# Kernel tuning notes

Measured on AMD Instinct MI355X. Metric: run time of the kernel, lower is better.

## Reference

```python
import jax, jax.numpy as jnp
import numpy as np

N_HIDDEN = 256
BATCH, T, N_FEAT = 256, 512, 64


def setup_inputs() -> dict:
    key = jax.random.key(0)
    ks = jax.random.split(key, 10)
    s = lambda fan_in: 1.0 / np.sqrt(fan_in)
    return {
        "x": jax.random.normal(ks[0], (BATCH, T, N_FEAT), dtype=jnp.float32),
        # input-side Dense gates (with bias)
        "Wr": jax.random.normal(ks[1], (N_FEAT, N_HIDDEN), dtype=jnp.float32) * s(N_FEAT),
        "br": jnp.zeros((N_HIDDEN,), dtype=jnp.float32),
        "Wz": jax.random.normal(ks[2], (N_FEAT, N_HIDDEN), dtype=jnp.float32) * s(N_FEAT),
        "bz": jnp.zeros((N_HIDDEN,), dtype=jnp.float32),
        "Wg": jax.random.normal(ks[3], (N_FEAT, N_HIDDEN), dtype=jnp.float32) * s(N_FEAT),
        "bg": jnp.zeros((N_HIDDEN,), dtype=jnp.float32),
        # hidden-side Dense gates (no bias)
        "Hr": jax.random.normal(ks[4], (N_HIDDEN, N_HIDDEN), dtype=jnp.float32) * s(N_HIDDEN),
        "Hz": jax.random.normal(ks[5], (N_HIDDEN, N_HIDDEN), dtype=jnp.float32) * s(N_HIDDEN),
        "Hg": jax.random.normal(ks[6], (N_HIDDEN, N_HIDDEN), dtype=jnp.float32) * s(N_HIDDEN),
    }


def _gru_forward(x, Wr, br, Wz, bz, Wg, bg, Hr, Hz, Hg):
    B, T, _ = x.shape
    nh = Hr.shape[0]
    # Source loops for t in range(T-1), so only x[:, :T-1] is consumed.
    xs = x[:, : T - 1]
    # Batch all input-side projections across time (parallel part).
    ar = jnp.einsum("btf,fh->tbh", xs, Wr) + br  # [T-1, B, H]
    az = jnp.einsum("btf,fh->tbh", xs, Wz) + bz
    ag = jnp.einsum("btf,fh->tbh", xs, Wg) + bg

    h0 = jnp.zeros((B, nh), dtype=x.dtype)

    def step(h, gates):
        gr, gz, gg = gates
        rt = jax.nn.sigmoid(gr + h @ Hr)
        zt = jax.nn.sigmoid(gz + h @ Hz)
        gt = jnp.tanh(gg + (rt * h) @ Hg)
        h_new = (1.0 - zt) * h + zt * gt
        return h_new, h_new

    _, hs = jax.lax.scan(step, h0, (ar, az, ag))  # hs: [T-1, B, H]
    # Output list starts with the zero initial state, matching the source.
    out = jnp.concatenate([h0[None], hs], axis=0)  # [T, B, H]
    return jnp.transpose(out, (1, 0, 2))  # [B, T, H]


def reference(x, Wr, br, Wz, bz, Wg, bg, Hr, Hz, Hg):
    return _gru_forward(x, Wr, br, Wz, bz, Wg, bg, Hr, Hz, Hg)
```

## Files before the change

kernel.cpp:

```cpp
#include <hip/hip_runtime.h>
#include <hip/hip_bf16.h>


typedef _Float16 f16;
typedef _Float16 half8 __attribute__((ext_vector_type(8)));
typedef float floatx4 __attribute__((ext_vector_type(4)));

#define MFMA16(a, b, c) __builtin_amdgcn_mfma_f32_16x16x32_f16((a), (b), (c), 0, 0, 0)

#define WTAB_OFF   0u
#define RZTAB_OFF  98304u
#define GTAB_OFF   360448u
#define PRE_OFF    491520u
#define WS_NEED    (491520ull + 200933376ull)

__global__ void gru_wprep(const float* __restrict__ Wr, const float* __restrict__ Wz,
                          const float* __restrict__ Wg, const float* __restrict__ Hr,
                          const float* __restrict__ Hz, const float* __restrict__ Hg,
                          f16* __restrict__ ws) {
    int idx = blockIdx.x * 256 + threadIdx.x;
    if (idx >= 30720) return;
    const float* src;
    int col, k0;
    f16* dst;
    if (idx < 6144) {
        int lane = idx & 63, ktx = (idx >> 6) & 1, nt = (idx >> 7) & 15, g = idx >> 11;
        src = (g == 0) ? Wr : (g == 1) ? Wz : Wg;
        col = nt * 16 + (lane & 15);
        k0  = ktx * 32 + (lane >> 4) * 8;
        dst = ws + WTAB_OFF / 2 + (size_t)idx * 8;
    } else if (idx < 22528) {
        int local = idx - 6144;
        int kt = local & 7, nti = (local >> 3) & 1, g = (local >> 4) & 1, tid = local >> 5;
        int w = tid >> 6, l = tid & 63;
        src = g ? Hz : Hr;
        col = (w * 2 + nti) * 16 + (l & 15);
        k0  = kt * 32 + (l >> 4) * 8;
        dst = ws + RZTAB_OFF / 2 + (size_t)local * 8;
    } else {
        int local = idx - 22528;
        int lane = local & 63, q = local >> 6;
        int kt = q & 7, nt = q >> 3;
        src = Hg;
        col = nt * 16 + (lane & 15);
        k0  = kt * 32 + (lane >> 4) * 8;
        dst = ws + GTAB_OFF / 2 + (size_t)local * 8;
    }
    half8 v;
#pragma unroll
    for (int i = 0; i < 8; ++i) v[i] = (f16)src[(size_t)(k0 + i) * 256 + col];
    *(half8*)dst = v;
}

__global__ void __launch_bounds__(512)
gru_gates(const float* __restrict__ x, const float* __restrict__ br,
          const float* __restrict__ bz, const float* __restrict__ bg,
          f16* __restrict__ ws) {
    const int bid = blockIdx.x;
    const int t = bid >> 4, blk = bid & 15;
    const int tid = threadIdx.x, w = tid >> 6, l = tid & 63;
    const int cl = l & 15, rq = l >> 4;

    half8 xa[2];
    const float* xr = x + (size_t)(blk * 16 + cl) * 32768 + (size_t)t * 64 + rq * 8;
#pragma unroll
    for (int ktx = 0; ktx < 2; ++ktx) {
        float4 a = *(const float4*)(xr + ktx * 32);
        float4 b = *(const float4*)(xr + ktx * 32 + 4);
        half8 v;
        v[0] = (f16)a.x; v[1] = (f16)a.y; v[2] = (f16)a.z; v[3] = (f16)a.w;
        v[4] = (f16)b.x; v[5] = (f16)b.y; v[6] = (f16)b.z; v[7] = (f16)b.w;
        xa[ktx] = v;
    }

    const half8* Wt = (const half8*)(ws + WTAB_OFF / 2);
    floatx4 acc[3][2];
#pragma unroll
    for (int g = 0; g < 3; ++g)
#pragma unroll
        for (int nti = 0; nti < 2; ++nti) {
            int col = (w * 2 + nti) * 16 + cl;
            float b = (g == 0 ? br : g == 1 ? bz : bg)[col];
            acc[g][nti] = (floatx4){b, b, b, b};
        }
#pragma unroll
    for (int g = 0; g < 3; ++g)
#pragma unroll
        for (int nti = 0; nti < 2; ++nti) {
            int nt = w * 2 + nti;
#pragma unroll
            for (int ktx = 0; ktx < 2; ++ktx)
                acc[g][nti] = MFMA16(xa[ktx], Wt[(size_t)((g * 16 + nt) * 2 + ktx) * 64 + l],
                                     acc[g][nti]);
        }

    half8* preb = (half8*)(ws + PRE_OFF / 2);
#pragma unroll
    for (int g = 0; g < 3; ++g) {
        half8 v;
#pragma unroll
        for (int nti = 0; nti < 2; ++nti)
#pragma unroll
            for (int j = 0; j < 4; ++j)
                v[nti * 4 + j] = (f16)acc[g][nti][j];
        preb[((size_t)bid * 3 + g) * 512 + tid] = v;
    }
}

__global__ void __launch_bounds__(512, 2)
gru_scan3(const f16* __restrict__ ws, float* __restrict__ out) {
    extern __shared__ unsigned char smem[];
    unsigned char* sH  = smem;
    unsigned char* sRH = smem + 8192;
    unsigned char* sG  = smem + 16384;

    const int tid = threadIdx.x, w = tid >> 6, l = tid & 63;
    const int cl = l & 15, rq = l >> 4;
    const int blk = blockIdx.x, b0 = blk * 16;

    half8 rz[2][2][8];
    {
        const half8* rzt = (const half8*)(ws + RZTAB_OFF / 2) + (size_t)tid * 32;
#pragma unroll
        for (int g = 0; g < 2; ++g)
#pragma unroll
            for (int nti = 0; nti < 2; ++nti)
#pragma unroll
                for (int kt = 0; kt < 8; ++kt)
                    rz[g][nti][kt] = rzt[g * 16 + nti * 8 + kt];
    }
#pragma unroll
    for (int g = 0; g < 2; ++g)
#pragma unroll
        for (int nti = 0; nti < 2; ++nti)
#pragma unroll
            for (int kt = 0; kt < 8; ++kt)
                asm volatile("" : "+v"(rz[g][nti][kt]));

    {
        const uint4* src = (const uint4*)(ws + GTAB_OFF / 2);
        uint4* dst = (uint4*)sG;
#pragma unroll
        for (int i = 0; i < 16; ++i) dst[tid + i * 512] = src[tid + i * 512];
    }
    { uint4 z = {}; ((uint4*)sH)[tid] = z; }
    for (int i = tid; i < 4096; i += 512) {
        int row = i >> 8, col = i & 255;
        out[(size_t)(b0 + row) * 131072 + col] = 0.f;
    }

    float h[2][4] = {};
    float zs[2][4];

    const half8* preb = (const half8*)(ws + PRE_OFF / 2);
    half8 ucur[3], unxt[3] = {};
#pragma unroll
    for (int g = 0; g < 3; ++g)
        ucur[g] = preb[((size_t)blk * 3 + g) * 512 + tid];

    asm volatile("s_waitcnt lgkmcnt(0)" ::: "memory");
    __builtin_amdgcn_s_barrier();
    __builtin_amdgcn_sched_barrier(0);

    const int abase = cl * 512;
    const int asw   = (cl & 7) << 4;

    for (int t = 0; t < 511; ++t) {
        if (t < 510) {
            const half8* p = preb + ((size_t)((t + 1) * 16 + blk) * 3) * 512 + tid;
#pragma unroll
            for (int g = 0; g < 3; ++g) unxt[g] = p[g * 512];
        }

        floatx4 aR[2] = {}, aZ[2] = {};
#pragma unroll
        for (int kt = 0; kt < 8; ++kt) {
            half8 av = *(const half8*)(sH + abase + ((kt * 64 + rq * 16) ^ asw));
#pragma unroll
            for (int nti = 0; nti < 2; ++nti) {
                aR[nti] = MFMA16(av, rz[0][nti][kt], aR[nti]);
                aZ[nti] = MFMA16(av, rz[1][nti][kt], aZ[nti]);
            }
        }

#pragma unroll
        for (int nti = 0; nti < 2; ++nti) {
            int col = (w * 2 + nti) * 16 + cl;
#pragma unroll
            for (int j = 0; j < 4; ++j) {
                int row = rq * 4 + j;
                int e = nti * 4 + j;
                float r = __builtin_amdgcn_rcpf(1.f + __expf(-(aR[nti][j] + (float)ucur[0][e])));
                float z = __builtin_amdgcn_rcpf(1.f + __expf(-(aZ[nti][j] + (float)ucur[1][e])));
                zs[nti][j] = z;
                *(f16*)(sRH + row * 512 + ((col * 2) ^ ((row & 7) << 4))) = (f16)(r * h[nti][j]);
            }
        }
        asm volatile("s_waitcnt lgkmcnt(0)" ::: "memory");
        __builtin_amdgcn_s_barrier();
        __builtin_amdgcn_sched_barrier(0);

        floatx4 aG[2] = {};
#pragma unroll
        for (int kt = 0; kt < 8; ++kt) {
            half8 av = *(const half8*)(sRH + abase + ((kt * 64 + rq * 16) ^ asw));
#pragma unroll
            for (int nti = 0; nti < 2; ++nti) {
                int nt = w * 2 + nti;
                half8 bf = *(const half8*)(sG + (size_t)((nt * 8 + kt) * 64 + l) * 16);
                aG[nti] = MFMA16(av, bf, aG[nti]);
            }
        }

#pragma unroll
        for (int nti = 0; nti < 2; ++nti) {
            int col = (w * 2 + nti) * 16 + cl;
#pragma unroll
            for (int j = 0; j < 4; ++j) {
                int row = rq * 4 + j;
                int e = nti * 4 + j;
                float ex = __expf(2.f * (aG[nti][j] + (float)ucur[2][e]));
                float g = 1.f - 2.f * __builtin_amdgcn_rcpf(ex + 1.f);
                float hn = h[nti][j] + zs[nti][j] * (g - h[nti][j]);
                h[nti][j] = hn;
                *(f16*)(sH + row * 512 + ((col * 2) ^ ((row & 7) << 4))) = (f16)hn;
                out[(size_t)(b0 + row) * 131072 + (size_t)(t + 1) * 256 + col] = hn;
            }
        }
#pragma unroll
        for (int g = 0; g < 3; ++g) ucur[g] = unxt[g];
        asm volatile("s_waitcnt lgkmcnt(0)" ::: "memory");
        __builtin_amdgcn_s_barrier();
        __builtin_amdgcn_sched_barrier(0);
    }
}

__global__ void gru_prep(const float* __restrict__ Wr, const float* __restrict__ Wz,
                         const float* __restrict__ Wg, const float* __restrict__ Hr,
                         const float* __restrict__ Hz, const float* __restrict__ Hg,
                         f16* __restrict__ B) {
    int idx = blockIdx.x * 256 + threadIdx.x;
    int lane = idx & 63;
    int rest = idx >> 6;
    int kt = rest % 10;
    rest /= 10;
    int nt = rest & 15;
    int g  = rest >> 4;
    if (g >= 3) return;
    const float* H = (g == 0) ? Hr : (g == 1) ? Hz : Hg;
    const float* W = (g == 0) ? Wr : (g == 1) ? Wz : Wg;
    int col   = nt * 16 + (lane & 15);
    int kbase = kt * 32 + (lane >> 4) * 8;
    half8 v;
#pragma unroll
    for (int i = 0; i < 8; ++i) {
        int k = kbase + i;
        float val = (k < 256) ? H[k * 256 + col] : W[(k - 256) * 256 + col];
        v[i] = (f16)val;
    }
    *(half8*)(B + (size_t)idx * 8) = v;
}

__global__ void __launch_bounds__(512, 1)
gru_scan(const float* __restrict__ x,
         const float* __restrict__ br, const float* __restrict__ bz,
         const float* __restrict__ bg,
         const f16* __restrict__ Bfrag,
         float* __restrict__ out) {
    __shared__ __align__(16) unsigned char sH[8192];
    __shared__ __align__(16) unsigned char sRH[8192];
    __shared__ __align__(16) unsigned char sX[2][2048];

    const int tid  = threadIdx.x;
    const int wave = tid >> 6;
    const int lane = tid & 63;
    const int cl   = lane & 15;
    const int rq   = lane >> 4;
    const int b0   = blockIdx.x * 16;
    const int nt0  = wave * 2, nt1 = wave * 2 + 1;
    const int col0 = nt0 * 16 + cl, col1 = nt1 * 16 + cl;

    const int abase = cl * 512;
    const int asw   = (cl & 7) << 4;

    const float bR0 = br[col0], bR1 = br[col1];
    const float bZ0 = bz[col0], bZ1 = bz[col1];
    const float bG0 = bg[col0], bG1 = bg[col1];

    const half8* Bb  = (const half8*)Bfrag;
    const half8* pR0 = Bb + (size_t)((0 * 16 + nt0) * 10) * 64 + lane;
    const half8* pR1 = Bb + (size_t)((0 * 16 + nt1) * 10) * 64 + lane;
    const half8* pZ0 = Bb + (size_t)((1 * 16 + nt0) * 10) * 64 + lane;
    const half8* pZ1 = Bb + (size_t)((1 * 16 + nt1) * 10) * 64 + lane;
    const half8* pG0 = Bb + (size_t)((2 * 16 + nt0) * 10) * 64 + lane;
    const half8* pG1 = Bb + (size_t)((2 * 16 + nt1) * 10) * 64 + lane;

    float h0_[4] = {0.f, 0.f, 0.f, 0.f};
    float h1_[4] = {0.f, 0.f, 0.f, 0.f};
    float zs0[4], zs1[4];

    { half8 zz = {}; *(half8*)(sH + tid * 16) = zz; }
    for (int i = tid; i < 16 * 256; i += 512) {
        int r = i >> 8, c = i & 255;
        out[((size_t)(b0 + r) * 512) * 256 + c] = 0.f;
    }
    {
        size_t xo = (size_t)(b0 + wave) * 32768 + lane;
        float a0 = x[xo], a1 = x[xo + (size_t)8 * 32768];
        *(f16*)(sX[0] + wave * 128       + ((lane * 2) ^ ((wave & 7) << 4))) = (f16)a0;
        *(f16*)(sX[0] + (wave + 8) * 128 + ((lane * 2) ^ ((wave & 7) << 4))) = (f16)a1;
    }
    __syncthreads();

    for (int t = 0; t < 511; ++t) {
        const int xb = t & 1;
        float xp0 = 0.f, xp1 = 0.f;
        if (t < 510) {
            size_t xo = (size_t)(b0 + wave) * 32768 + (size_t)(t + 1) * 64 + lane;
            xp0 = x[xo];
            xp1 = x[xo + (size_t)8 * 32768];
        }

        floatx4 aR0 = {0,0,0,0}, aR1 = {0,0,0,0}, aZ0 = {0,0,0,0}, aZ1 = {0,0,0,0};
        half8 xa0, xa1;
#pragma unroll
        for (int kt = 0; kt < 8; ++kt) {
            half8 av = *(const half8*)(sH + abase + ((kt * 64 + rq * 16) ^ asw));
            aR0 = MFMA16(av, pR0[kt * 64], aR0);
            aR1 = MFMA16(av, pR1[kt * 64], aR1);
            aZ0 = MFMA16(av, pZ0[kt * 64], aZ0);
            aZ1 = MFMA16(av, pZ1[kt * 64], aZ1);
        }
        xa0 = *(const half8*)(sX[xb] + cl * 128 + ((rq * 16) ^ asw));
        xa1 = *(const half8*)(sX[xb] + cl * 128 + ((64 + rq * 16) ^ asw));
        aR0 = MFMA16(xa0, pR0[8 * 64], aR0);  aR1 = MFMA16(xa0, pR1[8 * 64], aR1);
        aZ0 = MFMA16(xa0, pZ0[8 * 64], aZ0);  aZ1 = MFMA16(xa0, pZ1[8 * 64], aZ1);
        aR0 = MFMA16(xa1, pR0[9 * 64], aR0);  aR1 = MFMA16(xa1, pR1[9 * 64], aR1);
        aZ0 = MFMA16(xa1, pZ0[9 * 64], aZ0);  aZ1 = MFMA16(xa1, pZ1[9 * 64], aZ1);

        if (t < 510) {
            const int nb = xb ^ 1;
            *(f16*)(sX[nb] + wave * 128       + ((lane * 2) ^ ((wave & 7) << 4))) = (f16)xp0;
            *(f16*)(sX[nb] + (wave + 8) * 128 + ((lane * 2) ^ ((wave & 7) << 4))) = (f16)xp1;
        }

#pragma unroll
        for (int j = 0; j < 4; ++j) {
            const int row = rq * 4 + j;
            float r0 = 1.f / (1.f + __expf(-(aR0[j] + bR0)));
            float r1 = 1.f / (1.f + __expf(-(aR1[j] + bR1)));
            zs0[j]   = 1.f / (1.f + __expf(-(aZ0[j] + bZ0)));
            zs1[j]   = 1.f / (1.f + __expf(-(aZ1[j] + bZ1)));
            const int sw = (row & 7) << 4;
            *(f16*)(sRH + row * 512 + ((col0 * 2) ^ sw)) = (f16)(r0 * h0_[j]);
            *(f16*)(sRH + row * 512 + ((col1 * 2) ^ sw)) = (f16)(r1 * h1_[j]);
        }
        __syncthreads();

        floatx4 aG0 = {0,0,0,0}, aG1 = {0,0,0,0};
#pragma unroll
        for (int kt = 0; kt < 8; ++kt) {
            half8 av = *(const half8*)(sRH + abase + ((kt * 64 + rq * 16) ^ asw));
            aG0 = MFMA16(av, pG0[kt * 64], aG0);
            aG1 = MFMA16(av, pG1[kt * 64], aG1);
        }
        aG0 = MFMA16(xa0, pG0[8 * 64], aG0);  aG1 = MFMA16(xa0, pG1[8 * 64], aG1);
        aG0 = MFMA16(xa1, pG0[9 * 64], aG0);  aG1 = MFMA16(xa1, pG1[9 * 64], aG1);

#pragma unroll
        for (int j = 0; j < 4; ++j) {
            const int row = rq * 4 + j;
            float e0 = __expf(2.f * (aG0[j] + bG0));
            float g0 = 1.f - 2.f / (e0 + 1.f);
            float e1 = __expf(2.f * (aG1[j] + bG1));
            float g1 = 1.f - 2.f / (e1 + 1.f);
            float hn0 = h0_[j] + zs0[j] * (g0 - h0_[j]);
            float hn1 = h1_[j] + zs1[j] * (g1 - h1_[j]);
            h0_[j] = hn0;
            h1_[j] = hn1;
            const int sw = (row & 7) << 4;
            *(f16*)(sH + row * 512 + ((col0 * 2) ^ sw)) = (f16)hn0;
            *(f16*)(sH + row * 512 + ((col1 * 2) ^ sw)) = (f16)hn1;
            size_t ob = ((size_t)(b0 + row) * 512 + (t + 1)) * 256;
            out[ob + col0] = hn0;
            out[ob + col1] = hn1;
        }
        __syncthreads();
    }
}

extern "C" void kernel_launch(void* const* d_in, const int* in_sizes, int n_in,
                              void* d_out, int out_size, void* d_ws, size_t ws_size,
                              hipStream_t stream) {
    const float* x  = (const float*)d_in[0];
    const float* Wr = (const float*)d_in[1];
    const float* br = (const float*)d_in[2];
    const float* Wz = (const float*)d_in[3];
    const float* bz = (const float*)d_in[4];
    const float* Wg = (const float*)d_in[5];
    const float* bg = (const float*)d_in[6];
    const float* Hr = (const float*)d_in[7];
    const float* Hz = (const float*)d_in[8];
    const float* Hg = (const float*)d_in[9];
    float* out = (float*)d_out;

    if (ws_size >= WS_NEED) {
        f16* ws = (f16*)d_ws;
        gru_wprep<<<120, 256, 0, stream>>>(Wr, Wz, Wg, Hr, Hz, Hg, ws);
        gru_gates<<<511 * 16, 512, 0, stream>>>(x, br, bz, bg, ws);
        (void)hipFuncSetAttribute((const void*)gru_scan3,
                                  hipFuncAttributeMaxDynamicSharedMemorySize, 147456);
        gru_scan3<<<16, 512, 147456, stream>>>(ws, out);
    } else {
        f16* Bfrag = (f16*)d_ws;
        gru_prep<<<120, 256, 0, stream>>>(Wr, Wz, Wg, Hr, Hz, Hg, Bfrag);
        gru_scan<<<16, 512, 0, stream>>>(x, br, bz, bg, Bfrag, out);
    }
}
```

Baseline: 1.075 ms.

## Swap MFMA operand order so each lane owns contiguous columns; vectorize stores

Swaps the A/B operands of the MFMAs in the gates and scan kernels, so each lane's accumulator holds four consecutive hidden columns of one batch row instead of four rows of one column. This allows half4 LDS stores of the hidden state and float4 global stores of the output in place of scattered scalar stores. It also pins the recurrent weight fragments in AGPRs via asm constraints to relieve VGPR pressure. The transposed layout must stay consistent with the precomputed gate tables, and AGPR placement could add register moves before the MFMAs.

```diff
diff --git a/kernel.cpp b/kernel.cpp
--- a/kernel.cpp
+++ b/kernel.cpp
@@ -3,6 +3,7 @@
 
 
 typedef _Float16 f16;
+typedef _Float16 half4 __attribute__((ext_vector_type(4)));
 typedef _Float16 half8 __attribute__((ext_vector_type(8)));
 typedef float floatx4 __attribute__((ext_vector_type(4)));
 
@@ -59,10 +60,10 @@
     const int bid = blockIdx.x;
     const int t = bid >> 4, blk = bid & 15;
     const int tid = threadIdx.x, w = tid >> 6, l = tid & 63;
-    const int cl = l & 15, rq = l >> 4;
-
-    half8 xa[2];
-    const float* xr = x + (size_t)(blk * 16 + cl) * 32768 + (size_t)t * 64 + rq * 8;
+    const int m = l & 15, rq = l >> 4;
+
+    half8 xb[2];
+    const float* xr = x + (size_t)(blk * 16 + m) * 32768 + (size_t)t * 64 + rq * 8;
 #pragma unroll
     for (int ktx = 0; ktx < 2; ++ktx) {
         float4 a = *(const float4*)(xr + ktx * 32);
@@ -70,7 +71,7 @@
         half8 v;
         v[0] = (f16)a.x; v[1] = (f16)a.y; v[2] = (f16)a.z; v[3] = (f16)a.w;
         v[4] = (f16)b.x; v[5] = (f16)b.y; v[6] = (f16)b.z; v[7] = (f16)b.w;
-        xa[ktx] = v;
+        xb[ktx] = v;
     }
 
     const half8* Wt = (const half8*)(ws + WTAB_OFF / 2);
@@ -79,9 +80,9 @@
     for (int g = 0; g < 3; ++g)
 #pragma unroll
         for (int nti = 0; nti < 2; ++nti) {
-            int col = (w * 2 + nti) * 16 + cl;
-            float b = (g == 0 ? br : g == 1 ? bz : bg)[col];
-            acc[g][nti] = (floatx4){b, b, b, b};
+            int n0 = (w * 2 + nti) * 16 + rq * 4;
+            float4 bv = *(const float4*)((g == 0 ? br : g == 1 ? bz : bg) + n0);
+            acc[g][nti] = (floatx4){bv.x, bv.y, bv.z, bv.w};
         }
 #pragma unroll
     for (int g = 0; g < 3; ++g)
@@ -90,7 +91,7 @@
             int nt = w * 2 + nti;
 #pragma unroll
             for (int ktx = 0; ktx < 2; ++ktx)
-                acc[g][nti] = MFMA16(xa[ktx], Wt[(size_t)((g * 16 + nt) * 2 + ktx) * 64 + l],
+                acc[g][nti] = MFMA16(Wt[(size_t)((g * 16 + nt) * 2 + ktx) * 64 + l], xb[ktx],
                                      acc[g][nti]);
         }
 
@@ -107,35 +108,41 @@
     }
 }
 
+
+#define WLOAD6(kt) \
+    half8 hr_##kt##_0 = rzt[kt],      hr_##kt##_1 = rzt[8 + kt];  \
+    half8 hz_##kt##_0 = rzt[16 + kt], hz_##kt##_1 = rzt[24 + kt]; \
+    asm volatile("" : "+a"(hr_##kt##_0), "+a"(hr_##kt##_1), \
+                      "+a"(hz_##kt##_0), "+a"(hz_##kt##_1));
+
+#define PA6(kt) { \
+    half8 hv = *(const half8*)(sH + hbase + (((kt) * 64 + rq * 16) ^ hsw)); \
+    aR0 = MFMA16(hr_##kt##_0, hv, aR0);  aZ0 = MFMA16(hz_##kt##_0, hv, aZ0); \
+    aR1 = MFMA16(hr_##kt##_1, hv, aR1);  aZ1 = MFMA16(hz_##kt##_1, hv, aZ1); }
+
+#define PB6(kt) { \
+    half8 hv = *(const half8*)(sRH + hbase + (((kt) * 64 + rq * 16) ^ hsw)); \
+    half8 bf0 = *(const half8*)(sG + (size_t)(((nt0 * 8 + (kt)) * 64 + l)) * 16); \
+    half8 bf1 = *(const half8*)(sG + (size_t)(((nt1 * 8 + (kt)) * 64 + l)) * 16); \
+    aG0 = MFMA16(bf0, hv, aG0); \
+    aG1 = MFMA16(bf1, hv, aG1); }
+
 __global__ void __launch_bounds__(512, 2)
-gru_scan3(const f16* __restrict__ ws, float* __restrict__ out) {
-    extern __shared__ unsigned char smem[];
+gru_scan6(const f16* __restrict__ ws, float* __restrict__ out) {
+    extern __shared__ __align__(16) unsigned char smem[];
     unsigned char* sH  = smem;
     unsigned char* sRH = smem + 8192;
     unsigned char* sG  = smem + 16384;
 
     const int tid = threadIdx.x, w = tid >> 6, l = tid & 63;
-    const int cl = l & 15, rq = l >> 4;
+    const int m = l & 15, rq = l >> 4;
     const int blk = blockIdx.x, b0 = blk * 16;
-
-    half8 rz[2][2][8];
-    {
-        const half8* rzt = (const half8*)(ws + RZTAB_OFF / 2) + (size_t)tid * 32;
-#pragma unroll
-        for (int g = 0; g < 2; ++g)
-#pragma unroll
-            for (int nti = 0; nti < 2; ++nti)
-#pragma unroll
-                for (int kt = 0; kt < 8; ++kt)
-                    rz[g][nti][kt] = rzt[g * 16 + nti * 8 + kt];
-    }
-#pragma unroll
-    for (int g = 0; g < 2; ++g)
-#pragma unroll
-        for (int nti = 0; nti < 2; ++nti)
-#pragma unroll
-            for (int kt = 0; kt < 8; ++kt)
-                asm volatile("" : "+v"(rz[g][nti][kt]));
+    const int nt0 = w * 2, nt1 = w * 2 + 1;
+    const int n0a = nt0 * 16 + rq * 4;
+    const int n0b = nt1 * 16 + rq * 4;
+
+    const half8* rzt = (const half8*)(ws + RZTAB_OFF / 2) + (size_t)tid * 32;
+    WLOAD6(0) WLOAD6(1) WLOAD6(2) WLOAD6(3) WLOAD6(4) WLOAD6(5) WLOAD6(6) WLOAD6(7)
 
     {
         const uint4* src = (const uint4*)(ws + GTAB_OFF / 2);
@@ -144,9 +151,10 @@
         for (int i = 0; i < 16; ++i) dst[tid + i * 512] = src[tid + i * 512];
     }
     { uint4 z = {}; ((uint4*)sH)[tid] = z; }
-    for (int i = tid; i < 4096; i += 512) {
-        int row = i >> 8, col = i & 255;
-        out[(size_t)(b0 + row) * 131072 + col] = 0.f;
+#pragma unroll
+    for (int i = 0; i < 8; ++i) {
+        int q = i * 512 + tid;
+        out[(size_t)(b0 + (q >> 8)) * 131072 + (q & 255)] = 0.f;
     }
 
     float h[2][4] = {};
@@ -162,8 +170,10 @@
     __builtin_amdgcn_s_barrier();
     __builtin_amdgcn_sched_barrier(0);
 
-    const int abase = cl * 512;
-    const int asw   = (cl & 7) << 4;
+    const int hbase = m * 512;
+    const int hsw   = (m & 7) << 4;
+    const int wbA   = hbase + ((n0a * 2) ^ hsw);
+    const int wbB   = hbase + ((n0b * 2) ^ hsw);
 
     for (int t = 0; t < 511; ++t) {
         if (t < 510) {
@@ -172,60 +182,51 @@
             for (int g = 0; g < 3; ++g) unxt[g] = p[g * 512];
         }
 
-        floatx4 aR[2] = {}, aZ[2] = {};
-#pragma unroll
-        for (int kt = 0; kt < 8; ++kt) {
-            half8 av = *(const half8*)(sH + abase + ((kt * 64 + rq * 16) ^ asw));
-#pragma unroll
-            for (int nti = 0; nti < 2; ++nti) {
-                aR[nti] = MFMA16(av, rz[0][nti][kt], aR[nti]);
-                aZ[nti] = MFMA16(av, rz[1][nti][kt], aZ[nti]);
+        floatx4 aR0 = {}, aR1 = {}, aZ0 = {}, aZ1 = {};
+        PA6(0) PA6(1) PA6(2) PA6(3) PA6(4) PA6(5) PA6(6) PA6(7)
+
+        {
+            half4 p0, p1;
+#pragma unroll
+            for (int j = 0; j < 4; ++j) {
+                float r0 = __builtin_amdgcn_rcpf(1.f + __expf(-(aR0[j] + (float)ucur[0][j])));
+                float z0 = __builtin_amdgcn_rcpf(1.f + __expf(-(aZ0[j] + (float)ucur[1][j])));
+                float r1 = __builtin_amdgcn_rcpf(1.f + __expf(-(aR1[j] + (float)ucur[0][4 + j])));
+                float z1 = __builtin_amdgcn_rcpf(1.f + __expf(-(aZ1[j] + (float)ucur[1][4 + j])));
+                zs[0][j] = z0;  zs[1][j] = z1;
+                p0[j] = (f16)(r0 * h[0][j]);
+                p1[j] = (f16)(r1 * h[1][j]);
             }
-        }
-
-#pragma unroll
-        for (int nti = 0; nti < 2; ++nti) {
-            int col = (w * 2 + nti) * 16 + cl;
-#pragma unroll
-            for (int j = 0; j < 4; ++j) {
-                int row = rq * 4 + j;
-                int e = nti * 4 + j;
-                float r = __builtin_amdgcn_rcpf(1.f + __expf(-(aR[nti][j] + (float)ucur[0][e])));
-                float z = __builtin_amdgcn_rcpf(1.f + __expf(-(aZ[nti][j] + (float)ucur[1][e])));
-                zs[nti][j] = z;
-                *(f16*)(sRH + row * 512 + ((col * 2) ^ ((row & 7) << 4))) = (f16)(r * h[nti][j]);
-            }
+            *(half4*)(sRH + wbA) = p0;
+            *(half4*)(sRH + wbB) = p1;
         }
         asm volatile("s_waitcnt lgkmcnt(0)" ::: "memory");
         __builtin_amdgcn_s_barrier();
         __builtin_amdgcn_sched_barrier(0);
 
-        floatx4 aG[2] = {};
-#pragma unroll
-        for (int kt = 0; kt < 8; ++kt) {
-            half8 av = *(const half8*)(sRH + abase + ((kt * 64 + rq * 16) ^ asw));
-#pragma unroll
-            for (int nti = 0; nti < 2; ++nti) {
-                int nt = w * 2 + nti;
-                half8 bf = *(const half8*)(sG + (size_t)((nt * 8 + kt) * 64 + l) * 16);
-                aG[nti] = MFMA16(av, bf, aG[nti]);
+        floatx4 aG0 = {}, aG1 = {};
+        PB6(0) PB6(1) PB6(2) PB6(3) PB6(4) PB6(5) PB6(6) PB6(7)
+
+        {
+            half4 p0, p1;
+            float4 o0, o1;
+#pragma unroll
+            for (int j = 0; j < 4; ++j) {
+                float e0 = __expf(2.f * (aG0[j] + (float)ucur[2][j]));
+                float g0 = 1.f - 2.f * __builtin_amdgcn_rcpf(e0 + 1.f);
+                float e1 = __expf(2.f * (aG1[j] + (float)ucur[2][4 + j]));
+                float g1 = 1.f - 2.f * __builtin_amdgcn_rcpf(e1 + 1.f);
+                float hn0 = h[0][j] + zs[0][j] * (g0 - h[0][j]);
+                float hn1 = h[1][j] + zs[1][j] * (g1 - h[1][j]);
+                h[0][j] = hn0;  h[1][j] = hn1;
+                p0[j] = (f16)hn0;  p1[j] = (f16)hn1;
+                ((float*)&o0)[j] = hn0;  ((float*)&o1)[j] = hn1;
             }
-        }
-
-#pragma unroll
-        for (int nti = 0; nti < 2; ++nti) {
-            int col = (w * 2 + nti) * 16 + cl;
-#pragma unroll
-            for (int j = 0; j < 4; ++j) {
-                int row = rq * 4 + j;
-                int e = nti * 4 + j;
-                float ex = __expf(2.f * (aG[nti][j] + (float)ucur[2][e]));
-                float g = 1.f - 2.f * __builtin_amdgcn_rcpf(ex + 1.f);
-                float hn = h[nti][j] + zs[nti][j] * (g - h[nti][j]);
-                h[nti][j] = hn;
-                *(f16*)(sH + row * 512 + ((col * 2) ^ ((row & 7) << 4))) = (f16)hn;
-                out[(size_t)(b0 + row) * 131072 + (size_t)(t + 1) * 256 + col] = hn;
-            }
+            *(half4*)(sH + wbA) = p0;
+            *(half4*)(sH + wbB) = p1;
+            float* ob = out + (size_t)(b0 + m) * 131072 + (size_t)(t + 1) * 256;
+            *(float4*)(ob + n0a) = o0;
+            *(float4*)(ob + n0b) = o1;
         }
 #pragma unroll
         for (int g = 0; g < 3; ++g) ucur[g] = unxt[g];
@@ -408,9 +409,9 @@
         f16* ws = (f16*)d_ws;
         gru_wprep<<<120, 256, 0, stream>>>(Wr, Wz, Wg, Hr, Hz, Hg, ws);
         gru_gates<<<511 * 16, 512, 0, stream>>>(x, br, bz, bg, ws);
-        (void)hipFuncSetAttribute((const void*)gru_scan3,
+        (void)hipFuncSetAttribute((const void*)gru_scan6,
                                   hipFuncAttributeMaxDynamicSharedMemorySize, 147456);
-        gru_scan3<<<16, 512, 147456, stream>>>(ws, out);
+        gru_scan6<<<16, 512, 147456, stream>>>(ws, out);
     } else {
         f16* Bfrag = (f16*)d_ws;
         gru_prep<<<120, 256, 0, stream>>>(Wr, Wz, Wg, Hr, Hz, Hg, Bfrag);
```

Result: slower. 1.145 ms (+6.5%).

## Move Z-gate matmul into second phase with double-buffered hidden state

Applied to the files above, without the earlier changes.

Computes the update-gate (Z) MFMAs and sigmoid in the same phase as the candidate-gate matmul instead of before the first barrier, shortening the serial R-gate phase. The hidden-state shared buffer is double-buffered so the second phase can read h(t) while writing h(t+1). This adds 8 KB of shared memory and a second LDS read per k-tile in phase two.

```diff
diff --git a/kernel.cpp b/kernel.cpp
--- a/kernel.cpp
+++ b/kernel.cpp
@@ -108,11 +108,11 @@
 }
 
 __global__ void __launch_bounds__(512, 2)
-gru_scan3(const f16* __restrict__ ws, float* __restrict__ out) {
+gru_scan10(const f16* __restrict__ ws, float* __restrict__ out) {
     extern __shared__ unsigned char smem[];
-    unsigned char* sH  = smem;
-    unsigned char* sRH = smem + 8192;
-    unsigned char* sG  = smem + 16384;
+    unsigned char* sHB = smem;
+    unsigned char* sRH = smem + 16384;
+    unsigned char* sG  = smem + 24576;
 
     const int tid = threadIdx.x, w = tid >> 6, l = tid & 63;
     const int cl = l & 15, rq = l >> 4;
@@ -143,14 +143,13 @@
 #pragma unroll
         for (int i = 0; i < 16; ++i) dst[tid + i * 512] = src[tid + i * 512];
     }
-    { uint4 z = {}; ((uint4*)sH)[tid] = z; }
+    { uint4 z = {}; ((uint4*)sHB)[tid] = z; }
     for (int i = tid; i < 4096; i += 512) {
         int row = i >> 8, col = i & 255;
         out[(size_t)(b0 + row) * 131072 + col] = 0.f;
     }
 
     float h[2][4] = {};
-    float zs[2][4];
 
     const half8* preb = (const half8*)(ws + PRE_OFF / 2);
     half8 ucur[3], unxt[3] = {};
@@ -166,21 +165,22 @@
     const int asw   = (cl & 7) << 4;
 
     for (int t = 0; t < 511; ++t) {
+        const unsigned char* sHc = sHB + (t & 1) * 8192;
+        unsigned char*       sHn = sHB + ((t + 1) & 1) * 8192;
+
         if (t < 510) {
             const half8* p = preb + ((size_t)((t + 1) * 16 + blk) * 3) * 512 + tid;
 #pragma unroll
             for (int g = 0; g < 3; ++g) unxt[g] = p[g * 512];
         }
 
-        floatx4 aR[2] = {}, aZ[2] = {};
+        floatx4 aR[2] = {};
 #pragma unroll
         for (int kt = 0; kt < 8; ++kt) {
-            half8 av = *(const half8*)(sH + abase + ((kt * 64 + rq * 16) ^ asw));
-#pragma unroll
-            for (int nti = 0; nti < 2; ++nti) {
+            half8 av = *(const half8*)(sHc + abase + ((kt * 64 + rq * 16) ^ asw));
+#pragma unroll
+            for (int nti = 0; nti < 2; ++nti)
                 aR[nti] = MFMA16(av, rz[0][nti][kt], aR[nti]);
-                aZ[nti] = MFMA16(av, rz[1][nti][kt], aZ[nti]);
-            }
         }
 
 #pragma unroll
@@ -191,8 +191,6 @@
                 int row = rq * 4 + j;
                 int e = nti * 4 + j;
                 float r = __builtin_amdgcn_rcpf(1.f + __expf(-(aR[nti][j] + (float)ucur[0][e])));
-                float z = __builtin_amdgcn_rcpf(1.f + __expf(-(aZ[nti][j] + (float)ucur[1][e])));
-                zs[nti][j] = z;
                 *(f16*)(sRH + row * 512 + ((col * 2) ^ ((row & 7) << 4))) = (f16)(r * h[nti][j]);
             }
         }
@@ -200,15 +198,17 @@
         __builtin_amdgcn_s_barrier();
         __builtin_amdgcn_sched_barrier(0);
 
-        floatx4 aG[2] = {};
+        floatx4 aZ[2] = {}, aG[2] = {};
 #pragma unroll
         for (int kt = 0; kt < 8; ++kt) {
-            half8 av = *(const half8*)(sRH + abase + ((kt * 64 + rq * 16) ^ asw));
+            half8 avh = *(const half8*)(sHc + abase + ((kt * 64 + rq * 16) ^ asw));
+            half8 avr = *(const half8*)(sRH + abase + ((kt * 64 + rq * 16) ^ asw));
 #pragma unroll
             for (int nti = 0; nti < 2; ++nti) {
                 int nt = w * 2 + nti;
                 half8 bf = *(const half8*)(sG + (size_t)((nt * 8 + kt) * 64 + l) * 16);
-                aG[nti] = MFMA16(av, bf, aG[nti]);
+                aZ[nti] = MFMA16(avh, rz[1][nti][kt], aZ[nti]);
+                aG[nti] = MFMA16(avr, bf, aG[nti]);
             }
         }
 
@@ -219,11 +219,12 @@
             for (int j = 0; j < 4; ++j) {
                 int row = rq * 4 + j;
                 int e = nti * 4 + j;
+                float z = __builtin_amdgcn_rcpf(1.f + __expf(-(aZ[nti][j] + (float)ucur[1][e])));
                 float ex = __expf(2.f * (aG[nti][j] + (float)ucur[2][e]));
                 float g = 1.f - 2.f * __builtin_amdgcn_rcpf(ex + 1.f);
-                float hn = h[nti][j] + zs[nti][j] * (g - h[nti][j]);
+                float hn = h[nti][j] + z * (g - h[nti][j]);
                 h[nti][j] = hn;
-                *(f16*)(sH + row * 512 + ((col * 2) ^ ((row & 7) << 4))) = (f16)hn;
+                *(f16*)(sHn + row * 512 + ((col * 2) ^ ((row & 7) << 4))) = (f16)hn;
                 out[(size_t)(b0 + row) * 131072 + (size_t)(t + 1) * 256 + col] = hn;
             }
         }
@@ -408,9 +409,9 @@
         f16* ws = (f16*)d_ws;
         gru_wprep<<<120, 256, 0, stream>>>(Wr, Wz, Wg, Hr, Hz, Hg, ws);
         gru_gates<<<511 * 16, 512, 0, stream>>>(x, br, bz, bg, ws);
-        (void)hipFuncSetAttribute((const void*)gru_scan3,
-                                  hipFuncAttributeMaxDynamicSharedMemorySize, 147456);
-        gru_scan3<<<16, 512, 147456, stream>>>(ws, out);
+        (void)hipFuncSetAttribute((const void*)gru_scan10,
+                                  hipFuncAttributeMaxDynamicSharedMemorySize, 155648);
+        gru_scan10<<<16, 512, 155648, stream>>>(ws, out);
     } else {
         f16* Bfrag = (f16*)d_ws;
         gru_prep<<<120, 256, 0, stream>>>(Wr, Wz, Wg, Hr, Hz, Hg, Bfrag);
```

After: 1.142 ms. 1.06x slower.
